# Kernel optimization log

Measured on AMD Instinct MI355X. Metric: run time of the kernel, lower is better.

Reference implementation:

```python
import jax, jax.numpy as jnp
import numpy as np


def setup_inputs() -> dict:
    key = jax.random.key(0)
    ks = jax.random.split(key, 7)
    B, T, D_in, H, D_out = 512, 1024, 128, 512, 128
    s = lambda k, shp, fan: jax.random.normal(k, shp, jnp.float32) / np.sqrt(fan)
    return {
        "x": jax.random.normal(ks[0], (B, T, D_in), jnp.float32),
        "Wx": s(ks[1], (H, D_in), D_in),
        "bx": jnp.zeros((H,), jnp.float32),
        "Wh": s(ks[2], (H, H), H),
        "bh": jnp.zeros((H,), jnp.float32),
        "Wy": s(ks[3], (D_out, H), H),
        "by": jnp.zeros((D_out,), jnp.float32),
    }


def reference(x, Wx, bx, Wh, bh, Wy, by):
    # x: [B, T, D_in]. Hoist input projection into one big GEMM (same math).
    B, T, _ = x.shape
    H = Wh.shape[0]
    xp = jnp.einsum("btd,hd->bth", x, Wx) + bx + bh  # [B, T, H]

    def step(h, xp_t):
        h = jnp.tanh(xp_t + h @ Wh.T)
        return h, None

    h0 = jnp.zeros((B, H), x.dtype)
    h_T, _ = jax.lax.scan(step, h0, jnp.swapaxes(xp, 0, 1))  # scan over time
    y = h_T @ Wy.T + by  # [B, D_out]
    return y
```

## Files before the change

kernel.cpp:

```cpp
#include <hip/hip_runtime.h>

typedef __bf16 bf16x8 __attribute__((ext_vector_type(8)));
typedef unsigned short ushort8_t __attribute__((ext_vector_type(8)));
typedef float f32x4 __attribute__((ext_vector_type(4)));
typedef unsigned int uint4_t __attribute__((ext_vector_type(4)));

#define MFMA16(a,b,c) __builtin_amdgcn_mfma_f32_16x16x32_bf16((a),(b),(c),0,0,0)


__device__ unsigned short g_xp[(size_t)32 * 1024 * 256 * 32];

__device__ __forceinline__ unsigned short f2bf(float f) {
  unsigned int u = __float_as_uint(f);
  u += 0x7FFFu + ((u >> 16) & 1u);
  return (unsigned short)(u >> 16);
}
__device__ __forceinline__ bf16x8 pack8v(float4 a, float4 b) {
  ushort8_t u;
  u[0] = f2bf(a.x); u[1] = f2bf(a.y); u[2] = f2bf(a.z); u[3] = f2bf(a.w);
  u[4] = f2bf(b.x); u[5] = f2bf(b.y); u[6] = f2bf(b.z); u[7] = f2bf(b.w);
  return __builtin_bit_cast(bf16x8, u);
}
__device__ __forceinline__ bf16x8 pack8p(const float* __restrict__ s) {
  return pack8v(*(const float4*)s, *(const float4*)(s + 4));
}

__global__ void rnn_prep(const float* __restrict__ Wh, const float* __restrict__ bx,
                         const float* __restrict__ bh, void* __restrict__ ws) {
  int gid = blockIdx.x * 256 + threadIdx.x;
  if (blockIdx.x < 32) {
    int l = gid & 63, f = gid >> 6;
    int ktl = f >> 5, wcf = f & 31;
    int c = (wcf >> 3) * 128 + (wcf & 7) * 16 + (l & 15);
    int k = (12 + ktl) * 32 + (l >> 4) * 8;
    bf16x8 v = pack8p(Wh + (size_t)c * 512 + k);
    ((ushort8_t*)ws)[gid] = __builtin_bit_cast(ushort8_t, v);
  } else {
    int i = threadIdx.x * 2;
    float* bias = (float*)((char*)ws + 131072);
    bias[i] = bx[i] + bh[i];
    bias[i + 1] = bx[i + 1] + bh[i + 1];
  }
}

__global__ __launch_bounds__(256) void xp_gemm(const float* __restrict__ x,
                                               const float* __restrict__ Wx,
                                               const void* __restrict__ ws) {
  __shared__ alignas(16) char xs[65536];
  const int tid = threadIdx.x;
  const int w = tid >> 6, l = tid & 63, m = l & 15, kg = l >> 4;
  const int g = blockIdx.x & 31, tc = blockIdx.x >> 5;
  const int bb = g << 4, t0 = tc << 4;
  const int sw = (m & 7) << 4;

  bf16x8 bwx[4][8];
  float bias[8];
  const float* biasp = (const float*)((const char*)ws + 131072);
#pragma unroll
  for (int cf = 0; cf < 8; ++cf) {
    const int c = w * 128 + cf * 16 + m;
    bias[cf] = biasp[c];
#pragma unroll
    for (int kt = 0; kt < 4; ++kt)
      bwx[kt][cf] = pack8p(Wx + (size_t)c * 128 + kt * 32 + kg * 8);
  }

#pragma unroll
  for (int pass = 0; pass < 8; ++pass) {
    const int row = pass * 32 + (tid >> 3);
    const int mr = row >> 4, tr = row & 15;
    const float* src = x + ((size_t)(bb + mr) * 1024 + t0 + tr) * 128 + (tid & 7) * 16;
    const int wbase = tr * 4096 + mr * 256;
    const int swr = (mr & 7) << 4;
#pragma unroll
    for (int j = 0; j < 4; ++j) {
      float4 v = *(const float4*)(src + j * 4);
      unsigned short h0 = f2bf(v.x), h1 = f2bf(v.y), h2 = f2bf(v.z), h3 = f2bf(v.w);
      unsigned lo = (unsigned)h0 | ((unsigned)h1 << 16);
      unsigned hi = (unsigned)h2 | ((unsigned)h3 << 16);
      unsigned* dst = (unsigned*)(xs + wbase + (((tid & 7) * 32 + j * 8) ^ swr));
      dst[0] = lo; dst[1] = hi;
    }
  }
  __syncthreads();

  const int xE = m * 256 + (((kg << 4)) ^ (sw & 48)) + (sw & 64);
  const int xO = m * 256 + (((kg << 4)) ^ (sw & 48)) + (64 ^ (sw & 64));

  for (int t = 0; t < 16; ++t) {
    f32x4 acc[8];
#pragma unroll
    for (int cf = 0; cf < 8; ++cf) acc[cf] = (f32x4){0.f, 0.f, 0.f, 0.f};
#pragma unroll
    for (int kt = 0; kt < 4; ++kt) {
      bf16x8 a = *(const bf16x8*)(xs + t * 4096 + ((kt >> 1) << 7) + ((kt & 1) ? xO : xE));
#pragma unroll
      for (int cf = 0; cf < 8; ++cf) acc[cf] = MFMA16(a, bwx[kt][cf], acc[cf]);
    }
    unsigned dw[16];
#pragma unroll
    for (int cf = 0; cf < 8; ++cf) {
      float p0 = acc[cf][0] + bias[cf], p1 = acc[cf][1] + bias[cf];
      float p2 = acc[cf][2] + bias[cf], p3 = acc[cf][3] + bias[cf];
      dw[cf * 2]     = (unsigned)f2bf(p0) | ((unsigned)f2bf(p1) << 16);
      dw[cf * 2 + 1] = (unsigned)f2bf(p2) | ((unsigned)f2bf(p3) << 16);
    }
    uint4_t* dst = (uint4_t*)(g_xp + ((size_t)((g * 1024) + (t0 + t)) * 256 + tid) * 32);
#pragma unroll
    for (int j = 0; j < 4; ++j)
      dst[j] = (uint4_t){dw[4 * j], dw[4 * j + 1], dw[4 * j + 2], dw[4 * j + 3]};
  }
}

__global__ __launch_bounds__(256, 1) void rnn_scan(
    const float* __restrict__ Wh, const float* __restrict__ Wy,
    const float* __restrict__ by, const void* __restrict__ ws,
    float* __restrict__ out) {
  __shared__ alignas(16) char h_lds[32768];
  __shared__ alignas(16) char wh_lds[98304];

  const int tid = threadIdx.x;
  const int w = tid >> 6, l = tid & 63, m = l & 15, kg = l >> 4;
  const int g = blockIdx.x, bb = g << 4;
  const int sw = (m & 7) << 4;

#pragma unroll
  for (int j = 0; j < 24; ++j) {
    const int off = (j * 256 + tid) * 16;
    *(uint4_t*)(wh_lds + off) = *(const uint4_t*)((const char*)ws + off);
  }

  bf16x8 bw[12][8];
#pragma unroll
  for (int cf = 0; cf < 8; ++cf) {
    const int c = w * 128 + cf * 16 + m;
#pragma unroll
    for (int kt = 0; kt < 12; ++kt)
      bw[kt][cf] = pack8p(Wh + (size_t)c * 512 + kt * 32 + kg * 8);
  }

  const char* wsk15 = (const char*)ws + 98304 + (w * 8) * 1024 + l * 16;
  const char* whb = wh_lds + (w * 8) * 1024 + l * 16;

  const int hE = m * 1024 + ((kg << 4) ^ (sw & 48)) + (sw & 64);
  const int hO = m * 1024 + ((kg << 4) ^ (sw & 48)) + (64 ^ (sw & 64));

  int cblk[8], ca2[8];
#pragma unroll
  for (int cf = 0; cf < 8; ++cf) {
    const int c = w * 128 + cf * 16 + m;
    cblk[cf] = (c >> 6) << 7;
    ca2[cf] = 2 * (c & 63);
  }

  {
    uint4_t z = {0, 0, 0, 0};
#pragma unroll
    for (int j = 0; j < 4; ++j) *(uint4_t*)(h_lds + tid * 64 + j * 16) = z;
  }

  const char* xpb = (const char*)(g_xp + ((size_t)g * 1024 * 256 + tid) * 32);
  uint4_t xq0, xq1, xq2, xq3;
  {
    const uint4_t* p = (const uint4_t*)xpb;
    xq0 = p[0]; xq1 = p[1]; xq2 = p[2]; xq3 = p[3];
  }
  __syncthreads();

  for (int t = 0; t < 1024; ++t) {
    const int cur = t & 1;
    const char* hb = h_lds + (cur << 14);
    char* hn = h_lds + ((cur ^ 1) << 14);

    const int tn = (t < 1023) ? t + 1 : 1023;
    const uint4_t* pn = (const uint4_t*)(xpb + (size_t)tn * 16384);
    uint4_t nq0 = pn[0], nq1 = pn[1], nq2 = pn[2], nq3 = pn[3];

    f32x4 acc[8];
#pragma unroll
    for (int cf = 0; cf < 8; ++cf) {
      const uint4_t q = (cf < 2) ? xq0 : (cf < 4) ? xq1 : (cf < 6) ? xq2 : xq3;
      const unsigned dlo = q[(cf & 1) * 2], dhi = q[(cf & 1) * 2 + 1];
      acc[cf][0] = __uint_as_float(dlo << 16);
      acc[cf][1] = __uint_as_float(dlo & 0xffff0000u);
      acc[cf][2] = __uint_as_float(dhi << 16);
      acc[cf][3] = __uint_as_float(dhi & 0xffff0000u);
    }

#pragma unroll
    for (int kt = 0; kt < 12; ++kt) {
      bf16x8 a = *(const bf16x8*)(hb + ((kt >> 1) << 7) + ((kt & 1) ? hO : hE));
#pragma unroll
      for (int cf = 0; cf < 8; ++cf) acc[cf] = MFMA16(a, bw[kt][cf], acc[cf]);
    }
#pragma unroll
    for (int ktl = 0; ktl < 3; ++ktl) {
      const int kt = 12 + ktl;
      bf16x8 a = *(const bf16x8*)(hb + ((kt >> 1) << 7) + ((kt & 1) ? hO : hE));
#pragma unroll
      for (int cf = 0; cf < 8; ++cf) {
        bf16x8 b = *(const bf16x8*)(whb + ktl * 32768 + cf * 1024);
        acc[cf] = MFMA16(a, b, acc[cf]);
      }
    }
    {
      bf16x8 a = *(const bf16x8*)(hb + (7 << 7) + hO);
#pragma unroll
      for (int cf = 0; cf < 8; ++cf) {
        bf16x8 b = *(const bf16x8*)(wsk15 + cf * 1024);
        acc[cf] = MFMA16(a, b, acc[cf]);
      }
    }

#pragma unroll
    for (int cf = 0; cf < 8; ++cf) {
#pragma unroll
      for (int i = 0; i < 4; ++i) {
        const int r = kg * 4 + i;
        float e = __expf(2.f * acc[cf][i]);
        unsigned short hv = f2bf(1.f - 2.f / (e + 1.f));
        *(unsigned short*)(hn + r * 1024 + cblk[cf] + (ca2[cf] ^ ((r & 7) << 4))) = hv;
      }
    }
    __syncthreads();
    xq0 = nq0; xq1 = nq1; xq2 = nq2; xq3 = nq3;
  }

  f32x4 y0 = {0, 0, 0, 0}, y1 = {0, 0, 0, 0};
  const int c0 = w * 32 + m, c1 = w * 32 + 16 + m;
#pragma unroll
  for (int kt = 0; kt < 16; ++kt) {
    bf16x8 a = *(const bf16x8*)(h_lds + ((kt >> 1) << 7) + ((kt & 1) ? hO : hE));
    y0 = MFMA16(a, pack8p(Wy + (size_t)c0 * 512 + kt * 32 + kg * 8), y0);
    y1 = MFMA16(a, pack8p(Wy + (size_t)c1 * 512 + kt * 32 + kg * 8), y1);
  }
  const float b0 = by[c0], b1 = by[c1];
#pragma unroll
  for (int i = 0; i < 4; ++i) {
    const int r = kg * 4 + i;
    out[(size_t)(bb + r) * 128 + c0] = y0[i] + b0;
    out[(size_t)(bb + r) * 128 + c1] = y1[i] + b1;
  }
}

extern "C" void kernel_launch(void* const* d_in, const int* in_sizes, int n_in,
                              void* d_out, int out_size, void* d_ws, size_t ws_size,
                              hipStream_t stream) {
  const float* x  = (const float*)d_in[0];
  const float* Wx = (const float*)d_in[1];
  const float* bx = (const float*)d_in[2];
  const float* Wh = (const float*)d_in[3];
  const float* bh = (const float*)d_in[4];
  const float* Wy = (const float*)d_in[5];
  const float* by = (const float*)d_in[6];

  rnn_prep<<<33, 256, 0, stream>>>(Wh, bx, bh, d_ws);
  xp_gemm<<<2048, 256, 0, stream>>>(x, Wx, d_ws);
  rnn_scan<<<32, 256, 0, stream>>>(Wh, Wy, by, d_ws, (float*)d_out);
}
```

Baseline: 5.226 ms.

## Rebalance Wh storage between registers and LDS, single-buffer h with packed DPP writes

Removes the prep kernel and computes the fused bias inside the GEMM. In the scan, Wh k-tiles are split three ways: 12 live in registers (previously 12), 4 sit in LDS (previously 3), and none are read from global workspace (previously one tile per step). The h state becomes single-buffered, which needs an extra barrier before the write-back. Adjacent lanes' bf16 outputs are combined with DPP so each write stores 32 bits instead of 16, halving LDS store count. This trades a second barrier per step for fewer global loads and fewer LDS stores, and the larger register set carries some spill risk.

```diff
diff --git a/kernel.cpp b/kernel.cpp
--- a/kernel.cpp
+++ b/kernel.cpp
@@ -25,27 +25,10 @@
   return pack8v(*(const float4*)s, *(const float4*)(s + 4));
 }
 
-__global__ void rnn_prep(const float* __restrict__ Wh, const float* __restrict__ bx,
-                         const float* __restrict__ bh, void* __restrict__ ws) {
-  int gid = blockIdx.x * 256 + threadIdx.x;
-  if (blockIdx.x < 32) {
-    int l = gid & 63, f = gid >> 6;
-    int ktl = f >> 5, wcf = f & 31;
-    int c = (wcf >> 3) * 128 + (wcf & 7) * 16 + (l & 15);
-    int k = (12 + ktl) * 32 + (l >> 4) * 8;
-    bf16x8 v = pack8p(Wh + (size_t)c * 512 + k);
-    ((ushort8_t*)ws)[gid] = __builtin_bit_cast(ushort8_t, v);
-  } else {
-    int i = threadIdx.x * 2;
-    float* bias = (float*)((char*)ws + 131072);
-    bias[i] = bx[i] + bh[i];
-    bias[i + 1] = bx[i + 1] + bh[i + 1];
-  }
-}
-
 __global__ __launch_bounds__(256) void xp_gemm(const float* __restrict__ x,
                                                const float* __restrict__ Wx,
-                                               const void* __restrict__ ws) {
+                                               const float* __restrict__ bx,
+                                               const float* __restrict__ bh) {
   __shared__ alignas(16) char xs[65536];
   const int tid = threadIdx.x;
   const int w = tid >> 6, l = tid & 63, m = l & 15, kg = l >> 4;
@@ -55,11 +38,10 @@
 
   bf16x8 bwx[4][8];
   float bias[8];
-  const float* biasp = (const float*)((const char*)ws + 131072);
 #pragma unroll
   for (int cf = 0; cf < 8; ++cf) {
     const int c = w * 128 + cf * 16 + m;
-    bias[cf] = biasp[c];
+    bias[cf] = bx[c] + bh[c];
 #pragma unroll
     for (int kt = 0; kt < 4; ++kt)
       bwx[kt][cf] = pack8p(Wx + (size_t)c * 128 + kt * 32 + kg * 8);
@@ -75,17 +57,16 @@
 #pragma unroll
     for (int j = 0; j < 4; ++j) {
       float4 v = *(const float4*)(src + j * 4);
-      unsigned short h0 = f2bf(v.x), h1 = f2bf(v.y), h2 = f2bf(v.z), h3 = f2bf(v.w);
-      unsigned lo = (unsigned)h0 | ((unsigned)h1 << 16);
-      unsigned hi = (unsigned)h2 | ((unsigned)h3 << 16);
+      unsigned lo = (unsigned)f2bf(v.x) | ((unsigned)f2bf(v.y) << 16);
+      unsigned hi = (unsigned)f2bf(v.z) | ((unsigned)f2bf(v.w) << 16);
       unsigned* dst = (unsigned*)(xs + wbase + (((tid & 7) * 32 + j * 8) ^ swr));
       dst[0] = lo; dst[1] = hi;
     }
   }
   __syncthreads();
 
-  const int xE = m * 256 + (((kg << 4)) ^ (sw & 48)) + (sw & 64);
-  const int xO = m * 256 + (((kg << 4)) ^ (sw & 48)) + (64 ^ (sw & 64));
+  const int xE = m * 256 + ((kg << 4) ^ sw);
+  const int xO = xE ^ 64;
 
   for (int t = 0; t < 16; ++t) {
     f32x4 acc[8];
@@ -114,44 +95,40 @@
 
 __global__ __launch_bounds__(256, 1) void rnn_scan(
     const float* __restrict__ Wh, const float* __restrict__ Wy,
-    const float* __restrict__ by, const void* __restrict__ ws,
-    float* __restrict__ out) {
-  __shared__ alignas(16) char h_lds[32768];
-  __shared__ alignas(16) char wh_lds[98304];
+    const float* __restrict__ by, float* __restrict__ out) {
+  __shared__ alignas(16) char h_lds[16384];
+  __shared__ alignas(16) char wb_lds[131072];
 
   const int tid = threadIdx.x;
   const int w = tid >> 6, l = tid & 63, m = l & 15, kg = l >> 4;
   const int g = blockIdx.x, bb = g << 4;
-  const int sw = (m & 7) << 4;
-
-#pragma unroll
-  for (int j = 0; j < 24; ++j) {
-    const int off = (j * 256 + tid) * 16;
-    *(uint4_t*)(wh_lds + off) = *(const uint4_t*)((const char*)ws + off);
-  }
-
-  bf16x8 bw[12][8];
+
+#pragma unroll
+  for (int ktl = 0; ktl < 4; ++ktl)
+#pragma unroll
+    for (int cf = 0; cf < 8; ++cf) {
+      const int c = w * 128 + cf * 16 + m;
+      const int k = (8 + ktl) * 32 + kg * 8;
+      *(bf16x8*)(wb_lds + ((w * 32 + ktl * 8 + cf) * 64 + l) * 16) =
+          pack8p(Wh + (size_t)c * 512 + k);
+    }
+
+  bf16x8 bw[8][8];
+  bf16x8 bw2[4][8];
 #pragma unroll
   for (int cf = 0; cf < 8; ++cf) {
     const int c = w * 128 + cf * 16 + m;
 #pragma unroll
-    for (int kt = 0; kt < 12; ++kt)
+    for (int kt = 0; kt < 8; ++kt)
       bw[kt][cf] = pack8p(Wh + (size_t)c * 512 + kt * 32 + kg * 8);
-  }
-
-  const char* wsk15 = (const char*)ws + 98304 + (w * 8) * 1024 + l * 16;
-  const char* whb = wh_lds + (w * 8) * 1024 + l * 16;
-
-  const int hE = m * 1024 + ((kg << 4) ^ (sw & 48)) + (sw & 64);
-  const int hO = m * 1024 + ((kg << 4) ^ (sw & 48)) + (64 ^ (sw & 64));
-
-  int cblk[8], ca2[8];
-#pragma unroll
-  for (int cf = 0; cf < 8; ++cf) {
-    const int c = w * 128 + cf * 16 + m;
-    cblk[cf] = (c >> 6) << 7;
-    ca2[cf] = 2 * (c & 63);
-  }
+#pragma unroll
+    for (int ktl = 0; ktl < 4; ++ktl)
+      bw2[ktl][cf] = pack8p(Wh + (size_t)c * 512 + (12 + ktl) * 32 + kg * 8);
+  }
+
+  const int aE = m * 1024 + ((kg << 4) ^ ((m & 7) << 4));
+  const int aO = aE ^ 64;
+  const char* wbp = wb_lds + ((w * 32) * 64 + l) * 16;
 
   {
     uint4_t z = {0, 0, 0, 0};
@@ -161,17 +138,10 @@
 
   const char* xpb = (const char*)(g_xp + ((size_t)g * 1024 * 256 + tid) * 32);
   uint4_t xq0, xq1, xq2, xq3;
-  {
-    const uint4_t* p = (const uint4_t*)xpb;
-    xq0 = p[0]; xq1 = p[1]; xq2 = p[2]; xq3 = p[3];
-  }
+  { const uint4_t* p = (const uint4_t*)xpb; xq0 = p[0]; xq1 = p[1]; xq2 = p[2]; xq3 = p[3]; }
   __syncthreads();
 
   for (int t = 0; t < 1024; ++t) {
-    const int cur = t & 1;
-    const char* hb = h_lds + (cur << 14);
-    char* hn = h_lds + ((cur ^ 1) << 14);
-
     const int tn = (t < 1023) ? t + 1 : 1023;
     const uint4_t* pn = (const uint4_t*)(xpb + (size_t)tn * 16384);
     uint4_t nq0 = pn[0], nq1 = pn[1], nq2 = pn[2], nq3 = pn[3];
@@ -188,38 +158,46 @@
     }
 
 #pragma unroll
-    for (int kt = 0; kt < 12; ++kt) {
-      bf16x8 a = *(const bf16x8*)(hb + ((kt >> 1) << 7) + ((kt & 1) ? hO : hE));
+    for (int kt = 0; kt < 8; ++kt) {
+      bf16x8 a = *(const bf16x8*)(h_lds + ((kt & 1) ? aO : aE) + ((kt >> 1) << 7));
 #pragma unroll
       for (int cf = 0; cf < 8; ++cf) acc[cf] = MFMA16(a, bw[kt][cf], acc[cf]);
     }
 #pragma unroll
-    for (int ktl = 0; ktl < 3; ++ktl) {
-      const int kt = 12 + ktl;
-      bf16x8 a = *(const bf16x8*)(hb + ((kt >> 1) << 7) + ((kt & 1) ? hO : hE));
+    for (int ktl = 0; ktl < 4; ++ktl) {
+      const int kt = 8 + ktl;
+      bf16x8 a = *(const bf16x8*)(h_lds + ((kt & 1) ? aO : aE) + ((kt >> 1) << 7));
 #pragma unroll
       for (int cf = 0; cf < 8; ++cf) {
-        bf16x8 b = *(const bf16x8*)(whb + ktl * 32768 + cf * 1024);
+        bf16x8 b = *(const bf16x8*)(wbp + (ktl * 8 + cf) * 1024);
         acc[cf] = MFMA16(a, b, acc[cf]);
       }
     }
-    {
-      bf16x8 a = *(const bf16x8*)(hb + (7 << 7) + hO);
-#pragma unroll
-      for (int cf = 0; cf < 8; ++cf) {
-        bf16x8 b = *(const bf16x8*)(wsk15 + cf * 1024);
-        acc[cf] = MFMA16(a, b, acc[cf]);
-      }
-    }
-
-#pragma unroll
-    for (int cf = 0; cf < 8; ++cf) {
+#pragma unroll
+    for (int ktl = 0; ktl < 4; ++ktl) {
+      const int kt = 12 + ktl;
+      bf16x8 a = *(const bf16x8*)(h_lds + ((kt & 1) ? aO : aE) + ((kt >> 1) << 7));
+#pragma unroll
+      for (int cf = 0; cf < 8; ++cf) acc[cf] = MFMA16(a, bw2[ktl][cf], acc[cf]);
+    }
+
+    __syncthreads();
+
+#pragma unroll
+    for (int cf = 0; cf < 8; ++cf) {
+      const int cblk = (w * 2 + (cf >> 2)) << 7;
+      const int col2 = ((cf & 3) << 5) + 2 * m;
 #pragma unroll
       for (int i = 0; i < 4; ++i) {
-        const int r = kg * 4 + i;
         float e = __expf(2.f * acc[cf][i]);
-        unsigned short hv = f2bf(1.f - 2.f / (e + 1.f));
-        *(unsigned short*)(hn + r * 1024 + cblk[cf] + (ca2[cf] ^ ((r & 7) << 4))) = hv;
+        float hv = 1.f - 2.f / (e + 1.f);
+        unsigned u = (unsigned)f2bf(hv);
+        unsigned nb = (unsigned)__builtin_amdgcn_mov_dpp((int)u, 0xB1, 0xF, 0xF, true);
+        if (!(m & 1)) {
+          const int r = kg * 4 + i;
+          const int addr = r * 1024 + cblk + (col2 ^ ((r & 7) << 4));
+          *(unsigned*)(h_lds + addr) = u | (nb << 16);
+        }
       }
     }
     __syncthreads();
@@ -230,7 +208,7 @@
   const int c0 = w * 32 + m, c1 = w * 32 + 16 + m;
 #pragma unroll
   for (int kt = 0; kt < 16; ++kt) {
-    bf16x8 a = *(const bf16x8*)(h_lds + ((kt >> 1) << 7) + ((kt & 1) ? hO : hE));
+    bf16x8 a = *(const bf16x8*)(h_lds + ((kt & 1) ? aO : aE) + ((kt >> 1) << 7));
     y0 = MFMA16(a, pack8p(Wy + (size_t)c0 * 512 + kt * 32 + kg * 8), y0);
     y1 = MFMA16(a, pack8p(Wy + (size_t)c1 * 512 + kt * 32 + kg * 8), y1);
   }
@@ -254,7 +232,6 @@
   const float* Wy = (const float*)d_in[5];
   const float* by = (const float*)d_in[6];
 
-  rnn_prep<<<33, 256, 0, stream>>>(Wh, bx, bh, d_ws);
-  xp_gemm<<<2048, 256, 0, stream>>>(x, Wx, d_ws);
-  rnn_scan<<<32, 256, 0, stream>>>(Wh, Wy, by, d_ws, (float*)d_out);
-}
+  xp_gemm<<<2048, 256, 0, stream>>>(x, Wx, bx, bh);
+  rnn_scan<<<32, 256, 0, stream>>>(Wh, Wy, by, (float*)d_out);
+}
```

Result: faster. 5.017 ms (-4.0%).
